# Kernel optimization log

Measured on AMD Instinct MI355X. Metric: run time of the kernel, lower is better.

The kernel has to match this reference:

```python
import jax, jax.numpy as jnp
import numpy as np


def _sq_dist(q, k):
    # pairwise squared L2 distance: [B,H,L,D] x [B,H,M,D] -> [B,H,L,M]
    q2 = jnp.sum(q * q, axis=-1)[..., :, None]
    k2 = jnp.sum(k * k, axis=-1)[..., None, :]
    qk = jnp.einsum('bhld,bhmd->bhlm', q, k)
    return q2 + k2 - 2.0 * qk


def setup_inputs() -> dict:
    key = jax.random.key(0)
    k1, k2, k3 = jax.random.split(key, 3)
    B, H, L, D = 2, 8, 2048, 64
    query = jax.random.normal(k1, (B, H, L, D), dtype=jnp.float32)
    key_t = jax.random.normal(k2, (B, H, L, D), dtype=jnp.float32)
    mask = jnp.ones((B, L), dtype=jnp.float32)
    # mu param: normal(0, 0.5) * [0,1][:,None,None] -> first component zeroed
    mu = (jax.random.normal(k3, (2, H, D), dtype=jnp.float32) * 0.5
          * jnp.array([0.0, 1.0], dtype=jnp.float32)[:, None, None])
    pi = jnp.array([0.5, 0.5], dtype=jnp.float32)
    return {'query': query, 'key': key_t, 'mask': mask, 'mu': mu, 'pi': pi}


def reference(query, key, mask, mu, pi):
    D = query.shape[-1]
    var = D ** 0.5  # self.var = head_dim ** 0.5
    neg = 1e6 * (1.0 - mask[:, None, None, :])  # [B,1,1,L]
    pic = jnp.clip(pi, 0.0, 1.0)
    qk1 = (-0.5 / var) * _sq_dist(query, key - mu[0][None, :, None, :]) - neg
    qk2 = (-0.5 / var) * _sq_dist(query, key - mu[1][None, :, None, :]) - neg
    attn = jnp.exp(qk1) * pic[0] + jnp.exp(qk2) * pic[1]
    return attn / jnp.sum(attn, axis=-1, keepdims=True)
```

## Files before the change

### kernel.cpp

```cpp
#include <hip/hip_runtime.h>
#include <math.h>

#define B_ 2
#define H_ 8
#define L_ 2048
#define D_ 64
#define BM 16
#define NT 256
#define NBLK 32
#define L2E 1.4426950408889634f

typedef _Float16 half8 __attribute__((ext_vector_type(8)));
typedef __attribute__((ext_vector_type(4))) float f4;

#define MFMA16F(a, b, c) __builtin_amdgcn_mfma_f32_16x16x32_f16(a, b, c, 0, 0, 0)

struct LdsT {
  float muv[2][D_];
  float er0[BM], er1[BM];
  float red[4][BM];
};

__device__ inline half8 cvt8(const float4& a0, const float4& a1) {
  half8 r;
  r[0] = (_Float16)a0.x; r[1] = (_Float16)a0.y;
  r[2] = (_Float16)a0.z; r[3] = (_Float16)a0.w;
  r[4] = (_Float16)a1.x; r[5] = (_Float16)a1.y;
  r[6] = (_Float16)a1.z; r[7] = (_Float16)a1.w;
  return r;
}

__global__ __launch_bounds__(256) void prep_kernel(
    const float* __restrict__ k, const float* __restrict__ mask,
    const float* __restrict__ mu, float2* __restrict__ ck,
    half8* __restrict__ wf)
{
  int bh = blockIdx.x >> 3;
  int c  = (blockIdx.x & 7) * 256 + threadIdx.x;
  int b  = bh >> 3, h = bh & 7;
  const float s = -0.0625f;
  const float* kp  = k  + ((size_t)bh * L_ + c) * D_;
  const float* mu0 = mu + (size_t)h * D_;
  const float* mu1 = mu + (size_t)(H_ * D_) + (size_t)h * D_;
  float x[D_];
#pragma unroll
  for (int d = 0; d < D_; d += 4)
    *reinterpret_cast<float4*>(&x[d]) = *reinterpret_cast<const float4*>(kp + d);
  float s0 = 0.f, s1 = 0.f;
#pragma unroll
  for (int d = 0; d < D_; ++d) {
    float a = x[d] - mu0[d]; s0 += a * a;
    float bb = x[d] - mu1[d]; s1 += bb * bb;
  }
  float neg = 1.0e6f * (1.0f - mask[(size_t)b * L_ + c]);
  ck[(size_t)bh * L_ + c] = make_float2(exp2f((s * s0 - neg) * L2E),
                                        exp2f((s * s1 - neg) * L2E));
  int blk = c >> 4, ci = c & 15;
  half8* base = wf + ((size_t)bh * 128 + blk) * 128;
#pragma unroll
  for (int g = 0; g < 8; ++g) {
    int hh = g >> 2, kg = g & 3;
    base[hh * 64 + kg * 16 + ci] =
        cvt8(*reinterpret_cast<const float4*>(&x[8 * g]),
             *reinterpret_cast<const float4*>(&x[8 * g + 4]));
  }
}

template <bool USE_WS>
__global__ __launch_bounds__(NT, 8) void mg_kernel(
    const float* __restrict__ q, const float* __restrict__ kk,
    const float* __restrict__ mask, const float* __restrict__ mu,
    const float* __restrict__ pi, const float2* __restrict__ ckw,
    const half8* __restrict__ wf, float* __restrict__ out)
{
  __shared__ LdsT S;
  const int t = threadIdx.x;
  int bid = blockIdx.x;
  int vwg = (bid & 7) * 256 + (bid >> 3);
  int bh  = vwg >> 7;
  int rb  = vwg & 127;
  int b = bh >> 3, h = bh & 7;
  int row0 = rb * BM;

  const int w  = t >> 6;
  const int ln = t & 63;
  const int ci = ln & 15;
  const int kg = ln >> 4;

  const float s   = -0.0625f;
  const float DDC = 0.125f * L2E;

  const float*  maskb = mask + (size_t)b * L_;
  const float2* ckb   = ckw + (size_t)bh * L_;
  const half8*  wfb   = wf + (size_t)bh * (128 * 128);

  if (t < 2 * D_)
    S.muv[t >> 6][t & 63] =
        mu[(size_t)(t >> 6) * (H_ * D_) + (size_t)h * D_ + (t & 63)];

  half8 ah[2];
  {
    const float* qrow = q + ((size_t)bh * L_ + row0 + ci) * D_;
#pragma unroll
    for (int h2 = 0; h2 < 2; ++h2) {
      float4 a0 = *reinterpret_cast<const float4*>(qrow + 32 * h2 + kg * 8);
      float4 a1 = *reinterpret_cast<const float4*>(qrow + 32 * h2 + kg * 8 + 4);
      ah[h2] = cvt8(a0, a1);
    }
  }
  __syncthreads();

  if (t < BM) {
    float pi0 = fminf(fmaxf(pi[0], 0.f), 1.f);
    float pi1 = fminf(fmaxf(pi[1], 0.f), 1.f);
    const float* qr = q + ((size_t)bh * L_ + row0 + t) * D_;
    float a0 = 0.f, a1 = 0.f, a2 = 0.f;
#pragma unroll
    for (int dq = 0; dq < 16; ++dq) {
      float4 qv = *reinterpret_cast<const float4*>(qr + 4 * dq);
      a0 += qv.x * qv.x + qv.y * qv.y + qv.z * qv.z + qv.w * qv.w;
      a1 += qv.x * S.muv[0][4*dq] + qv.y * S.muv[0][4*dq+1] +
            qv.z * S.muv[0][4*dq+2] + qv.w * S.muv[0][4*dq+3];
      a2 += qv.x * S.muv[1][4*dq] + qv.y * S.muv[1][4*dq+1] +
            qv.z * S.muv[1][4*dq+2] + qv.w * S.muv[1][4*dq+3];
    }
    S.er0[t] = pi0 * exp2f((s * a0 + 2.f * s * a1) * L2E);
    S.er1[t] = pi1 * exp2f((s * a0 + 2.f * s * a2) * L2E);
  }
  __syncthreads();

  float e0r[4], e1r[4];
#pragma unroll
  for (int reg = 0; reg < 4; ++reg) {
    e0r[reg] = S.er0[kg * 4 + reg];
    e1r[reg] = S.er1[kg * 4 + reg];
  }

  auto LOADCOL = [&](int blk, half8& b0, half8& b1, float2& ec) {
    if (USE_WS) {
      const half8* pb = wfb + (size_t)blk * 128;
      b0 = pb[ln];
      b1 = pb[64 + ln];
      ec = ckb[blk * 16 + ci];
    } else {
      int col = blk * 16 + ci;
      const float* kp = kk + ((size_t)bh * L_ + col) * D_;
      float4 x0 = *reinterpret_cast<const float4*>(kp + 8 * kg);
      float4 x1 = *reinterpret_cast<const float4*>(kp + 8 * kg + 4);
      float4 x2 = *reinterpret_cast<const float4*>(kp + 32 + 8 * kg);
      float4 x3 = *reinterpret_cast<const float4*>(kp + 32 + 8 * kg + 4);
      b0 = cvt8(x0, x1);
      b1 = cvt8(x2, x3);
      int d0 = 8 * kg, d1 = 32 + 8 * kg;
      float s0 = 0.f, s1 = 0.f;
      float xs[8] = {x0.x, x0.y, x0.z, x0.w, x1.x, x1.y, x1.z, x1.w};
      float ys[8] = {x2.x, x2.y, x2.z, x2.w, x3.x, x3.y, x3.z, x3.w};
#pragma unroll
      for (int i = 0; i < 8; ++i) {
        float a;
        a = xs[i] - S.muv[0][d0 + i]; s0 += a * a;
        a = xs[i] - S.muv[1][d0 + i]; s1 += a * a;
        a = ys[i] - S.muv[0][d1 + i]; s0 += a * a;
        a = ys[i] - S.muv[1][d1 + i]; s1 += a * a;
      }
      s0 += __shfl_xor(s0, 16, 64); s0 += __shfl_xor(s0, 32, 64);
      s1 += __shfl_xor(s1, 16, 64); s1 += __shfl_xor(s1, 32, 64);
      float neg = 1.0e6f * (1.0f - maskb[col]);
      ec = make_float2(exp2f((s * s0 - neg) * L2E),
                       exp2f((s * s1 - neg) * L2E));
    }
  };

  float rsum[4] = {0.f, 0.f, 0.f, 0.f};
  const int blkw = w * NBLK;
#pragma unroll 4
  for (int j = 0; j < NBLK; ++j) {
    half8 b0, b1; float2 ec;
    LOADCOL(blkw + j, b0, b1, ec);
    f4 acc = {0.f, 0.f, 0.f, 0.f};
    acc = MFMA16F(ah[0], b0, acc);
    acc = MFMA16F(ah[1], b1, acc);
#pragma unroll
    for (int reg = 0; reg < 4; ++reg) {
      float g2 = __builtin_amdgcn_exp2f(DDC * acc[reg]);
      float m  = fmaf(e0r[reg], ec.x, e1r[reg] * ec.y);
      rsum[reg] = fmaf(g2, m, rsum[reg]);
    }
  }

#pragma unroll
  for (int reg = 0; reg < 4; ++reg) {
    float v = rsum[reg];
    v += __shfl_xor(v, 1, 64);
    v += __shfl_xor(v, 2, 64);
    v += __shfl_xor(v, 4, 64);
    v += __shfl_xor(v, 8, 64);
    if (ci == 0) S.red[w][kg * 4 + reg] = v;
  }
  __syncthreads();
#pragma unroll
  for (int reg = 0; reg < 4; ++reg) {
    int r = kg * 4 + reg;
    float inv = 1.0f / (S.red[0][r] + S.red[1][r] + S.red[2][r] + S.red[3][r]);
    e0r[reg] *= inv;
    e1r[reg] *= inv;
  }

  float* ob = out + ((size_t)bh * L_ + row0 + kg * 4) * L_ + w * 512 + ci;
#pragma unroll 4
  for (int j = 0; j < NBLK; ++j) {
    half8 b0, b1; float2 ec;
    LOADCOL(blkw + j, b0, b1, ec);
    f4 acc = {0.f, 0.f, 0.f, 0.f};
    acc = MFMA16F(ah[0], b0, acc);
    acc = MFMA16F(ah[1], b1, acc);
#pragma unroll
    for (int reg = 0; reg < 4; ++reg) {
      float g2 = __builtin_amdgcn_exp2f(DDC * acc[reg]);
      float m  = fmaf(e0r[reg], ec.x, e1r[reg] * ec.y);
      float p  = g2 * m;
      __builtin_nontemporal_store(p, ob + (size_t)reg * L_ + j * 16);
    }
  }
}

extern "C" void kernel_launch(void* const* d_in, const int* in_sizes, int n_in,
                              void* d_out, int out_size, void* d_ws, size_t ws_size,
                              hipStream_t stream) {
  const float* q    = (const float*)d_in[0];
  const float* k    = (const float*)d_in[1];
  const float* mask = (const float*)d_in[2];
  const float* mu   = (const float*)d_in[3];
  const float* pi   = (const float*)d_in[4];
  float* out = (float*)d_out;

  const size_t ck_bytes = (size_t)B_ * H_ * L_ * sizeof(float2);
  const size_t wp_bytes = (size_t)B_ * H_ * L_ * D_ * sizeof(short);
  const bool use_ws = (ws_size >= ck_bytes + wp_bytes) && (d_ws != nullptr);

  if (use_ws) {
    float2* ck = (float2*)d_ws;
    half8*  wf = (half8*)((char*)d_ws + ck_bytes);
    prep_kernel<<<dim3(B_ * H_ * 8), dim3(256), 0, stream>>>(k, mask, mu, ck, wf);
    mg_kernel<true><<<dim3(B_ * H_ * (L_ / BM)), dim3(NT), 0, stream>>>(
        q, k, mask, mu, pi, ck, wf, out);
  } else {
    mg_kernel<false><<<dim3(B_ * H_ * (L_ / BM)), dim3(NT), 0, stream>>>(
        q, k, mask, mu, pi, nullptr, nullptr, out);
  }
}
```

Baseline: 99.38 us.

## Split prep kernel across 8 threads per key row and prefetch next column block

The prep kernel now assigns eight threads per key row, each loading 8 floats. The per-row squared-distance sums are combined with cross-lane shuffles, and each thread writes one half8. This replaces a single thread holding a 64-float array, raising parallelism and reducing register pressure in that small launch. Both main loops in mg_kernel also software-prefetch the next column block's fp16 key fragments and exp terms before doing the MFMA on the current one, to hide load latency. The prefetch adds registers and could reduce occupancy.

```diff
diff --git a/kernel.cpp b/kernel.cpp
--- a/kernel.cpp
+++ b/kernel.cpp
@@ -35,35 +35,35 @@
     const float* __restrict__ mu, float2* __restrict__ ck,
     half8* __restrict__ wf)
 {
-  int bh = blockIdx.x >> 3;
-  int c  = (blockIdx.x & 7) * 256 + threadIdx.x;
-  int b  = bh >> 3, h = bh & 7;
+  int u   = blockIdx.x * 256 + threadIdx.x;
+  int col = u >> 3;
+  int g   = u & 7;
+  int bh  = col >> 11, c = col & 2047;
+  int b   = bh >> 3,   h = bh & 7;
   const float s = -0.0625f;
-  const float* kp  = k  + ((size_t)bh * L_ + c) * D_;
-  const float* mu0 = mu + (size_t)h * D_;
-  const float* mu1 = mu + (size_t)(H_ * D_) + (size_t)h * D_;
-  float x[D_];
-#pragma unroll
-  for (int d = 0; d < D_; d += 4)
-    *reinterpret_cast<float4*>(&x[d]) = *reinterpret_cast<const float4*>(kp + d);
+  const float* kp  = k + (((size_t)bh * L_ + c) * D_) + 8 * g;
+  const float* mu0 = mu + (size_t)h * D_ + 8 * g;
+  const float* mu1 = mu + (size_t)(H_ * D_) + (size_t)h * D_ + 8 * g;
+  float4 x0 = *reinterpret_cast<const float4*>(kp);
+  float4 x1 = *reinterpret_cast<const float4*>(kp + 4);
+  float xs[8] = {x0.x, x0.y, x0.z, x0.w, x1.x, x1.y, x1.z, x1.w};
   float s0 = 0.f, s1 = 0.f;
 #pragma unroll
-  for (int d = 0; d < D_; ++d) {
-    float a = x[d] - mu0[d]; s0 += a * a;
-    float bb = x[d] - mu1[d]; s1 += bb * bb;
-  }
-  float neg = 1.0e6f * (1.0f - mask[(size_t)b * L_ + c]);
-  ck[(size_t)bh * L_ + c] = make_float2(exp2f((s * s0 - neg) * L2E),
-                                        exp2f((s * s1 - neg) * L2E));
+  for (int i = 0; i < 8; ++i) {
+    float a;
+    a = xs[i] - mu0[i]; s0 += a * a;
+    a = xs[i] - mu1[i]; s1 += a * a;
+  }
+  s0 += __shfl_xor(s0, 1, 64); s0 += __shfl_xor(s0, 2, 64); s0 += __shfl_xor(s0, 4, 64);
+  s1 += __shfl_xor(s1, 1, 64); s1 += __shfl_xor(s1, 2, 64); s1 += __shfl_xor(s1, 4, 64);
+  if (g == 0) {
+    float neg = 1.0e6f * (1.0f - mask[(size_t)b * L_ + c]);
+    ck[(size_t)bh * L_ + c] = make_float2(exp2f((s * s0 - neg) * L2E),
+                                          exp2f((s * s1 - neg) * L2E));
+  }
   int blk = c >> 4, ci = c & 15;
-  half8* base = wf + ((size_t)bh * 128 + blk) * 128;
-#pragma unroll
-  for (int g = 0; g < 8; ++g) {
-    int hh = g >> 2, kg = g & 3;
-    base[hh * 64 + kg * 16 + ci] =
-        cvt8(*reinterpret_cast<const float4*>(&x[8 * g]),
-             *reinterpret_cast<const float4*>(&x[8 * g + 4]));
-  }
+  wf[((size_t)bh * 128 + blk) * 128 + (g >> 2) * 64 + (g & 3) * 16 + ci] =
+      cvt8(x0, x1);
 }
 
 template <bool USE_WS>
@@ -173,18 +173,23 @@
 
   float rsum[4] = {0.f, 0.f, 0.f, 0.f};
   const int blkw = w * NBLK;
-#pragma unroll 4
-  for (int j = 0; j < NBLK; ++j) {
+  {
     half8 b0, b1; float2 ec;
-    LOADCOL(blkw + j, b0, b1, ec);
-    f4 acc = {0.f, 0.f, 0.f, 0.f};
-    acc = MFMA16F(ah[0], b0, acc);
-    acc = MFMA16F(ah[1], b1, acc);
-#pragma unroll
-    for (int reg = 0; reg < 4; ++reg) {
-      float g2 = __builtin_amdgcn_exp2f(DDC * acc[reg]);
-      float m  = fmaf(e0r[reg], ec.x, e1r[reg] * ec.y);
-      rsum[reg] = fmaf(g2, m, rsum[reg]);
+    LOADCOL(blkw, b0, b1, ec);
+#pragma unroll 2
+    for (int j = 0; j < NBLK; ++j) {
+      half8 nb0, nb1; float2 nec;
+      if (j + 1 < NBLK) LOADCOL(blkw + j + 1, nb0, nb1, nec);
+      f4 acc = {0.f, 0.f, 0.f, 0.f};
+      acc = MFMA16F(ah[0], b0, acc);
+      acc = MFMA16F(ah[1], b1, acc);
+#pragma unroll
+      for (int reg = 0; reg < 4; ++reg) {
+        float g2 = __builtin_amdgcn_exp2f(DDC * acc[reg]);
+        float m  = fmaf(e0r[reg], ec.x, e1r[reg] * ec.y);
+        rsum[reg] = fmaf(g2, m, rsum[reg]);
+      }
+      b0 = nb0; b1 = nb1; ec = nec;
     }
   }
 
@@ -207,19 +212,24 @@
   }
 
   float* ob = out + ((size_t)bh * L_ + row0 + kg * 4) * L_ + w * 512 + ci;
-#pragma unroll 4
-  for (int j = 0; j < NBLK; ++j) {
+  {
     half8 b0, b1; float2 ec;
-    LOADCOL(blkw + j, b0, b1, ec);
-    f4 acc = {0.f, 0.f, 0.f, 0.f};
-    acc = MFMA16F(ah[0], b0, acc);
-    acc = MFMA16F(ah[1], b1, acc);
-#pragma unroll
-    for (int reg = 0; reg < 4; ++reg) {
-      float g2 = __builtin_amdgcn_exp2f(DDC * acc[reg]);
-      float m  = fmaf(e0r[reg], ec.x, e1r[reg] * ec.y);
-      float p  = g2 * m;
-      __builtin_nontemporal_store(p, ob + (size_t)reg * L_ + j * 16);
+    LOADCOL(blkw, b0, b1, ec);
+#pragma unroll 2
+    for (int j = 0; j < NBLK; ++j) {
+      half8 nb0, nb1; float2 nec;
+      if (j + 1 < NBLK) LOADCOL(blkw + j + 1, nb0, nb1, nec);
+      f4 acc = {0.f, 0.f, 0.f, 0.f};
+      acc = MFMA16F(ah[0], b0, acc);
+      acc = MFMA16F(ah[1], b1, acc);
+#pragma unroll
+      for (int reg = 0; reg < 4; ++reg) {
+        float g2 = __builtin_amdgcn_exp2f(DDC * acc[reg]);
+        float m  = fmaf(e0r[reg], ec.x, e1r[reg] * ec.y);
+        float p  = g2 * m;
+        __builtin_nontemporal_store(p, ob + (size_t)reg * L_ + j * 16);
+      }
+      b0 = nb0; b1 = nb1; ec = nec;
     }
   }
 }
@@ -241,7 +251,8 @@
   if (use_ws) {
     float2* ck = (float2*)d_ws;
     half8*  wf = (half8*)((char*)d_ws + ck_bytes);
-    prep_kernel<<<dim3(B_ * H_ * 8), dim3(256), 0, stream>>>(k, mask, mu, ck, wf);
+    prep_kernel<<<dim3(B_ * H_ * L_ * 8 / 256), dim3(256), 0, stream>>>(
+        k, mask, mu, ck, wf);
     mg_kernel<true><<<dim3(B_ * H_ * (L_ / BM)), dim3(NT), 0, stream>>>(
         q, k, mask, mu, pi, ck, wf, out);
   } else {
```

Measured after the change: 175.6 us. +76.7%, slower.
